# Performance work log

Measured on AMD Instinct MI355X. Metric: run time of the kernel, lower is better.

The kernel has to match this reference:

```python
import jax, jax.numpy as jnp
import numpy as np
import math

B, T1, T2, T3, D = 8, 32, 32, 16, 512
L, DL = 20, 128


def setup_inputs() -> dict:
    key = jax.random.key(0)
    ks = jax.random.split(key, 16)
    s = lambda fan: 1.0 / math.sqrt(fan)
    return {
        "f_c": jax.random.normal(ks[0], (B, T1, T2, T3, D), jnp.float32),
        "f_w": jax.random.normal(ks[1], (B, L, D), jnp.float32),
        "f_s": jax.random.normal(ks[2], (B, D), jnp.float32),
        "f_m": jax.random.normal(ks[3], (B, T1, T2, D), jnp.float32),
        "Wc_down": jax.random.normal(ks[4], (DL, D), jnp.float32) * s(D),
        "bc_down": jnp.zeros((DL,), jnp.float32),
        "Ww": jax.random.normal(ks[5], (DL, D), jnp.float32) * s(D),
        "bw": jnp.zeros((DL,), jnp.float32),
        "Ws": jax.random.normal(ks[6], (DL, D), jnp.float32) * s(D),
        "bs": jnp.zeros((DL,), jnp.float32),
        "Wq": jax.random.normal(ks[7], (DL, DL), jnp.float32) * s(DL),
        "bq": jnp.zeros((DL,), jnp.float32),
        "Wk": jax.random.normal(ks[8], (DL, DL), jnp.float32) * s(DL),
        "bk": jnp.zeros((DL,), jnp.float32),
        "Wc_up": jax.random.normal(ks[9], (D, DL), jnp.float32) * s(DL),
        "bc_up": jnp.zeros((D,), jnp.float32),
    }


def reference(f_c, f_w, f_s, f_m, Wc_down, bc_down, Ww, bw, Ws, bs,
              Wq, bq, Wk, bk, Wc_up, bc_up):
    inv_sqrt_dl = 1.0 / math.sqrt(DL)
    # 1x1 conv projections == per-position linear layers
    f_c_hat = jnp.einsum('bxyzd,ld->bxyzl', f_c, Wc_down) + bc_down  # [B,T1,T2,T3,dl]
    f_w_hat = f_w @ Ww.T + bw                                        # [B,L,dl]
    f_s_hat = f_s @ Ws.T + bs                                        # [B,dl]
    # Content attention: query from map, key/value from words
    q = f_c_hat @ Wq.T + bq                                          # [B,T1,T2,T3,dl]
    k = f_w_hat @ Wk.T + bk                                          # [B,L,dl]
    scores = jnp.einsum('bxyzd,bld->bxyzl', q, k) * inv_sqrt_dl
    attn = jax.nn.softmax(scores, axis=-1)
    f_caq = jnp.einsum('bxyzl,bld->bxyzd', attn, f_w_hat)            # [B,T1,T2,T3,dl]
    # Gate with sentence feature
    f_cq = f_c_hat * (f_caq + f_s_hat[:, None, None, None, :])
    # Self-attention over last spatial axis (T3)
    A_c = jnp.einsum('bxyzd,bxywd->bxyzw', f_cq, f_cq) * inv_sqrt_dl  # [B,T1,T2,T3,T3]
    A_c = jax.nn.softmax(A_c, axis=-1)
    f_cc_hat = jnp.einsum('bxyzw,bxywd->bxyzd', A_c, f_c_hat)
    f_cc = jnp.einsum('bxyzl,dl->bxyzd', f_cc_hat, Wc_up) + bc_up     # [B,T1,T2,T3,D]
    # Sigmoid gating residual for f_m
    g_m = jax.nn.sigmoid(f_m * f_s[:, None, None, :])
    fbar_m = g_m * f_m                                                # [B,T1,T2,D]
    return f_cc + f_c + fbar_m[:, :, :, None, :]
```

## Files before the change

### kernel.cpp

```cpp
#include <hip/hip_runtime.h>
#include <math.h>

#define B_ 8
#define T1_ 32
#define T2_ 32
#define T3_ 16
#define D_ 512
#define L_ 20
#define DL_ 128
#define M_ (B_*T1_*T2_*T3_)

#define WS_FW   0
#define WS_KQ   20480
#define WS_FS   40960
#define WS_SB   41984
#define WS_WDB  42144
#define WS_WUB  74912

typedef __attribute__((ext_vector_type(8))) short short8_t;
typedef __attribute__((ext_vector_type(4))) float f32x4;

__device__ __forceinline__ unsigned short f2b(float f) {
  unsigned int u = __float_as_uint(f);
  return (unsigned short)((u + 0x7fffu + ((u >> 16) & 1u)) >> 16);
}
__device__ __forceinline__ float b2f(short s) {
  return __uint_as_float(((unsigned)(unsigned short)s) << 16);
}
__device__ __forceinline__ int4 pack8(float4 a, float4 b) {
  int4 p;
  p.x = (int)f2b(a.x) | ((int)f2b(a.y) << 16);
  p.y = (int)f2b(a.z) | ((int)f2b(a.w) << 16);
  p.z = (int)f2b(b.x) | ((int)f2b(b.y) << 16);
  p.w = (int)f2b(b.z) | ((int)f2b(b.w) << 16);
  return p;
}

__global__ __launch_bounds__(256) void k0_convert(
    const float* __restrict__ Wd, const float* __restrict__ Wu,
    unsigned short* __restrict__ wdb, unsigned short* __restrict__ wub) {
  int g = blockIdx.x * 256 + threadIdx.x;
  if (g < 16384) {
    float4 v = ((const float4*)Wd)[g];
    ushort4 h; h.x = f2b(v.x); h.y = f2b(v.y); h.z = f2b(v.z); h.w = f2b(v.w);
    ((ushort4*)wdb)[g] = h;
  } else {
    int q = g - 16384;
    float4 v = ((const float4*)Wu)[q];
    ushort4 h; h.x = f2b(v.x); h.y = f2b(v.y); h.z = f2b(v.z); h.w = f2b(v.w);
    ((ushort4*)wub)[q] = h;
  }
}

__global__ __launch_bounds__(128) void k1_small(
    const float* __restrict__ f_w, const float* __restrict__ f_s,
    const float* __restrict__ Ww, const float* __restrict__ bw,
    const float* __restrict__ Ws, const float* __restrict__ bs,
    const float* __restrict__ Wq, const float* __restrict__ bq,
    const float* __restrict__ Wk, const float* __restrict__ bk,
    float* __restrict__ ws) {
  const int bl = blockIdx.x;
  const int b = bl / L_, l = bl % L_;
  const int d = threadIdx.x;
  __shared__ float s_fw[DL_];
  __shared__ float s_k[DL_];
  {
    const float* x = f_w + (size_t)(b*L_+l)*D_;
    const float* w = Ww + (size_t)d*D_;
    float acc = 0.f;
    for (int i = 0; i < D_; i += 4)
      acc += x[i]*w[i] + x[i+1]*w[i+1] + x[i+2]*w[i+2] + x[i+3]*w[i+3];
    acc += bw[d];
    s_fw[d] = acc;
    ws[WS_FW + (b*L_+l)*DL_ + d] = acc;
  }
  if (l == 0) {
    const float* x = f_s + (size_t)b*D_;
    const float* w = Ws + (size_t)d*D_;
    float acc = 0.f;
    for (int i = 0; i < D_; i += 4)
      acc += x[i]*w[i] + x[i+1]*w[i+1] + x[i+2]*w[i+2] + x[i+3]*w[i+3];
    ws[WS_FS + b*DL_ + d] = acc + bs[d];
  }
  __syncthreads();
  {
    const float* w = Wk + (size_t)d*DL_;
    float acc = 0.f;
    for (int i = 0; i < DL_; ++i) acc += s_fw[i]*w[i];
    s_k[d] = acc + bk[d];
  }
  __syncthreads();
  {
    float acc = 0.f;
    for (int c = 0; c < DL_; ++c) acc += s_k[c] * Wq[c*DL_ + d];
    ws[WS_KQ + (b*L_+l)*DL_ + d] = acc;
  }
  if (d == 0) {
    float acc = 0.f;
    for (int c = 0; c < DL_; ++c) acc += bq[c]*s_k[c];
    ws[WS_SB + b*L_ + l] = acc;
  }
}

#define SFCH_B 0
#define FCQ_B  8192
#define WD_B   16384
#define FC_B   32768
#define KQ_B   16384
#define FW_B   21824
#define FS_B   27264
#define SB_B   27776
#define ATTN_B 27904
#define AC_B   30592
#define WU_B   16384
#define SMEM_B 36864

__global__ __launch_bounds__(256, 4) void k2_fused(
    const float* __restrict__ f_c, const unsigned short* __restrict__ wdb,
    const unsigned short* __restrict__ wub,
    const float* __restrict__ bc_down, const float* __restrict__ bc_up,
    const float* __restrict__ f_m, const float* __restrict__ f_s,
    const float* __restrict__ ws, float* __restrict__ out) {
  __shared__ __align__(16) char smb[SMEM_B];
  float* sAttn = (float*)(smb + ATTN_B);
  float* sAc   = (float*)(smb + AC_B);
  float* sFs   = (float*)(smb + FS_B);
  float* sSb   = (float*)(smb + SB_B);

  const int t = threadIdx.x;
  const int row0 = blockIdx.x * 32;
  const int b = row0 >> 14;
  const int lane = t & 63, w = t >> 6;
  const int l15 = lane & 15, l4 = lane >> 4;
  const int wr = (w & 1) * 16;
  const int wc = w >> 1;
  const float inv_sqrt_dl = 0.08838834764831843f;
  const f32x4 z4 = {0.f, 0.f, 0.f, 0.f};
  const int sd_r = t >> 3, sd_k8 = (t & 7) * 8;

  f32x4 dacc[4];
  #pragma unroll
  for (int cf = 0; cf < 4; ++cf) dacc[cf] = z4;

  for (int kc = 0; kc < D_; kc += 64) {
    #pragma unroll
    for (int i = 0; i < 4; ++i) {
      int idx = t + i*256;
      int d = idx >> 3, kb = idx & 7;
      *(int4*)(smb + WD_B + d*128 + ((kb*16) ^ ((d & 7) << 4))) =
        *(const int4*)(wdb + (size_t)d*D_ + kc + kb*8);
    }
    {
      const float* src = f_c + (size_t)(row0 + sd_r)*D_ + kc + sd_k8;
      float4 v0 = *(const float4*)src;
      float4 v1 = *(const float4*)(src + 4);
      int4 pk = pack8(v0, v1);
      *(int4*)(smb + FC_B + sd_r*128 + ((sd_k8*2) ^ ((sd_r & 7) << 4))) = pk;
    }
    __syncthreads();
    #pragma unroll
    for (int ks = 0; ks < 2; ++ks) {
      const int rr = wr + l15;
      short8_t bfrag = *(const short8_t*)(smb + FC_B + rr*128 +
                        ((ks*64 + l4*16) ^ ((rr & 7) << 4)));
      #pragma unroll
      for (int cf = 0; cf < 4; ++cf) {
        const int d = wc*64 + cf*16 + l15;
        short8_t afrag = *(const short8_t*)(smb + WD_B + d*128 +
                          ((ks*64 + l4*16) ^ ((d & 7) << 4)));
        dacc[cf] = __builtin_amdgcn_mfma_f32_16x16x32_bf16(afrag, bfrag, dacc[cf], 0, 0, 0);
      }
    }
    __syncthreads();
  }
  {
    const int rr = wr + l15;
    const int rs = (rr & 7) << 4;
    #pragma unroll
    for (int cf = 0; cf < 4; ++cf) {
      const int d0 = wc*64 + cf*16 + l4*4;
      float4 bias = *(const float4*)(bc_down + d0);
      ushort4 pk;
      pk.x = f2b(dacc[cf][0] + bias.x); pk.y = f2b(dacc[cf][1] + bias.y);
      pk.z = f2b(dacc[cf][2] + bias.z); pk.w = f2b(dacc[cf][3] + bias.w);
      *(ushort4*)(smb + SFCH_B + rr*256 + ((d0*2) ^ rs)) = pk;
    }
  }
  for (int p = t; p < L_*16; p += 256) {
    const int l = p >> 4, c8 = (p & 15) * 8;
    float4 a0 = *(const float4*)(ws + WS_KQ + (b*L_+l)*DL_ + c8);
    float4 a1 = *(const float4*)(ws + WS_KQ + (b*L_+l)*DL_ + c8 + 4);
    *(int4*)(smb + KQ_B + l*272 + c8*2) = pack8(a0, a1);
    float4 b0 = *(const float4*)(ws + WS_FW + (b*L_+l)*DL_ + c8);
    float4 b1 = *(const float4*)(ws + WS_FW + (b*L_+l)*DL_ + c8 + 4);
    *(int4*)(smb + FW_B + l*272 + c8*2) = pack8(b0, b1);
  }
  if (t < 32) *(float4*)(sFs + t*4) = *(const float4*)(ws + WS_FS + b*DL_ + t*4);
  if (t < L_) sSb[t] = ws[WS_SB + b*L_ + t];
  __syncthreads();

  for (int p = t; p < 32*L_; p += 256) {
    const int r = p / L_, l = p - r*L_;
    const int qs = (r & 7) << 4;
    const char* qrow = smb + SFCH_B + r*256;
    const short* kr = (const short*)(smb + KQ_B + l*272);
    float s = 0.f;
    #pragma unroll
    for (int k = 0; k < DL_; k += 8) {
      short8_t qv = *(const short8_t*)(qrow + ((k*2) ^ qs));
      short8_t kv = *(const short8_t*)(kr + k);
      s += b2f(qv[0])*b2f(kv[0]) + b2f(qv[1])*b2f(kv[1])
         + b2f(qv[2])*b2f(kv[2]) + b2f(qv[3])*b2f(kv[3])
         + b2f(qv[4])*b2f(kv[4]) + b2f(qv[5])*b2f(kv[5])
         + b2f(qv[6])*b2f(kv[6]) + b2f(qv[7])*b2f(kv[7]);
    }
    sAttn[r*21 + l] = (s + sSb[l]) * inv_sqrt_dl;
  }
  __syncthreads();
  if (t < 32) {
    float* srow = sAttn + t*21;
    float m = -1e30f;
    for (int l = 0; l < L_; ++l) m = fmaxf(m, srow[l]);
    float sum = 0.f;
    for (int l = 0; l < L_; ++l) { float e = __expf(srow[l]-m); srow[l] = e; sum += e; }
    float inv = 1.f/sum;
    for (int l = 0; l < L_; ++l) srow[l] *= inv;
  }
  __syncthreads();
  for (int p = t; p < 1024; p += 256) {
    const int r = p >> 5, d4 = (p & 31) * 4;
    float ax = 0.f, ay = 0.f, az = 0.f, aw = 0.f;
    for (int l = 0; l < L_; ++l) {
      float a = sAttn[r*21 + l];
      ushort4 wv = *(const ushort4*)(smb + FW_B + l*272 + d4*2);
      ax += a*b2f((short)wv.x); ay += a*b2f((short)wv.y);
      az += a*b2f((short)wv.z); aw += a*b2f((short)wv.w);
    }
    const int rs = (r & 7) << 4;
    float4 fs4 = *(const float4*)(sFs + d4);
    ushort4 fh = *(const ushort4*)(smb + SFCH_B + r*256 + ((d4*2) ^ rs));
    ushort4 pk;
    pk.x = f2b(b2f((short)fh.x)*(ax+fs4.x));
    pk.y = f2b(b2f((short)fh.y)*(ay+fs4.y));
    pk.z = f2b(b2f((short)fh.z)*(az+fs4.z));
    pk.w = f2b(b2f((short)fh.w)*(aw+fs4.w));
    *(ushort4*)(smb + FCQ_B + r*256 + ((d4*2) ^ rs)) = pk;
  }
  __syncthreads();
  for (int p = t; p < 512; p += 256) {
    const int g = p >> 8, z = (p >> 4) & 15, wq = p & 15;
    const int xr = g*16 + z, yr = g*16 + wq;
    const char* xb = smb + FCQ_B + xr*256;
    const char* yb = smb + FCQ_B + yr*256;
    const int xs = (xr & 7) << 4, ys = (yr & 7) << 4;
    float s = 0.f;
    #pragma unroll
    for (int k = 0; k < DL_; k += 8) {
      short8_t xv = *(const short8_t*)(xb + ((k*2) ^ xs));
      short8_t yv = *(const short8_t*)(yb + ((k*2) ^ ys));
      s += b2f(xv[0])*b2f(yv[0]) + b2f(xv[1])*b2f(yv[1])
         + b2f(xv[2])*b2f(yv[2]) + b2f(xv[3])*b2f(yv[3])
         + b2f(xv[4])*b2f(yv[4]) + b2f(xv[5])*b2f(yv[5])
         + b2f(xv[6])*b2f(yv[6]) + b2f(xv[7])*b2f(yv[7]);
    }
    sAc[(g*16+z)*17 + wq] = s * inv_sqrt_dl;
  }
  __syncthreads();
  if (t < 32) {
    float* srow = sAc + t*17;
    float m = -1e30f;
    for (int wq = 0; wq < 16; ++wq) m = fmaxf(m, srow[wq]);
    float sum = 0.f;
    for (int wq = 0; wq < 16; ++wq) { float e = __expf(srow[wq]-m); srow[wq] = e; sum += e; }
    float inv = 1.f/sum;
    for (int wq = 0; wq < 16; ++wq) srow[wq] *= inv;
  }
  __syncthreads();
  for (int p = t; p < 1024; p += 256) {
    const int r = p >> 5, d4 = (p & 31)*4;
    const int g = r >> 4, z = r & 15;
    float ax = 0.f, ay = 0.f, az = 0.f, aw = 0.f;
    #pragma unroll
    for (int wq = 0; wq < 16; ++wq) {
      float a = sAc[(g*16+z)*17 + wq];
      const int fr = g*16 + wq;
      ushort4 fv = *(const ushort4*)(smb + SFCH_B + fr*256 + ((d4*2) ^ ((fr & 7) << 4)));
      ax += a*b2f((short)fv.x); ay += a*b2f((short)fv.y);
      az += a*b2f((short)fv.z); aw += a*b2f((short)fv.w);
    }
    ushort4 pk;
    pk.x = f2b(ax); pk.y = f2b(ay); pk.z = f2b(az); pk.w = f2b(aw);
    *(ushort4*)(smb + FCQ_B + r*256 + ((d4*2) ^ ((r & 7) << 4))) = pk;
  }
  __syncthreads();

  const int rr = wr + l15;
  const char* fcqrow = smb + FCQ_B + rr*256;
  const int xsw = (rr & 7) << 4;
  const int grow = row0 + rr;
  const size_t obase = (size_t)grow * D_;
  const size_t mbase = (size_t)(grow >> 4) * D_;
  for (int ch = 0; ch < 8; ++ch) {
    #pragma unroll
    for (int i = 0; i < 4; ++i) {
      int idx = t + i*256;
      int d = idx >> 4, kb = idx & 15;
      *(int4*)(smb + WU_B + d*256 + ((kb*16) ^ ((d & 7) << 4))) =
        *(const int4*)(wub + (size_t)(ch*64 + d)*DL_ + kb*8);
    }
    __syncthreads();
    f32x4 uacc[2]; uacc[0] = z4; uacc[1] = z4;
    #pragma unroll
    for (int ks = 0; ks < 4; ++ks) {
      short8_t bfrag = *(const short8_t*)(fcqrow + ((ks*64 + l4*16) ^ xsw));
      #pragma unroll
      for (int cf = 0; cf < 2; ++cf) {
        const int dd = wc*32 + cf*16 + l15;
        short8_t afrag = *(const short8_t*)(smb + WU_B + dd*256 +
                          ((ks*64 + l4*16) ^ ((dd & 7) << 4)));
        uacc[cf] = __builtin_amdgcn_mfma_f32_16x16x32_bf16(afrag, bfrag, uacc[cf], 0, 0, 0);
      }
    }
    #pragma unroll
    for (int cf = 0; cf < 2; ++cf) {
      const int d0 = ch*64 + wc*32 + cf*16 + l4*4;
      float4 bias = *(const float4*)(bc_up + d0);
      float4 fs4 = *(const float4*)(f_s + (size_t)b*D_ + d0);
      float4 fm4 = *(const float4*)(f_m + mbase + d0);
      float4 fc4 = *(const float4*)(f_c + obase + d0);
      float4 o;
      o.x = uacc[cf][0] + bias.x + fc4.x + fm4.x/(1.f + __expf(-fm4.x*fs4.x));
      o.y = uacc[cf][1] + bias.y + fc4.y + fm4.y/(1.f + __expf(-fm4.y*fs4.y));
      o.z = uacc[cf][2] + bias.z + fc4.z + fm4.z/(1.f + __expf(-fm4.z*fs4.z));
      o.w = uacc[cf][3] + bias.w + fc4.w + fm4.w/(1.f + __expf(-fm4.w*fs4.w));
      *(float4*)(out + obase + d0) = o;
    }
    __syncthreads();
  }
}

extern "C" void kernel_launch(void* const* d_in, const int* in_sizes, int n_in,
                              void* d_out, int out_size, void* d_ws, size_t ws_size,
                              hipStream_t stream) {
  (void)in_sizes; (void)n_in; (void)out_size; (void)ws_size;
  const float* f_c     = (const float*)d_in[0];
  const float* f_w     = (const float*)d_in[1];
  const float* f_s     = (const float*)d_in[2];
  const float* f_m     = (const float*)d_in[3];
  const float* Wc_down = (const float*)d_in[4];
  const float* bc_down = (const float*)d_in[5];
  const float* Ww      = (const float*)d_in[6];
  const float* bw      = (const float*)d_in[7];
  const float* Ws      = (const float*)d_in[8];
  const float* bs      = (const float*)d_in[9];
  const float* Wq      = (const float*)d_in[10];
  const float* bq      = (const float*)d_in[11];
  const float* Wk      = (const float*)d_in[12];
  const float* bk      = (const float*)d_in[13];
  const float* Wc_up   = (const float*)d_in[14];
  const float* bc_up   = (const float*)d_in[15];
  float* out = (float*)d_out;
  float* wsf = (float*)d_ws;
  unsigned short* wdb = (unsigned short*)(wsf + WS_WDB);
  unsigned short* wub = (unsigned short*)(wsf + WS_WUB);

  hipLaunchKernelGGL(k0_convert, dim3(128), dim3(256), 0, stream,
                     Wc_down, Wc_up, wdb, wub);
  hipLaunchKernelGGL(k1_small, dim3(B_*L_), dim3(128), 0, stream,
                     f_w, f_s, Ww, bw, Ws, bs, Wq, bq, Wk, bk, wsf);
  hipLaunchKernelGGL(k2_fused, dim3(M_/32), dim3(256), 0, stream,
                     f_c, wdb, wub, bc_down, bc_up, f_m, f_s, wsf, out);
}
```

Before: 269.6 us.

## Move attention score, context and self-attention matmuls onto MFMA with register softmax

Replaces the scalar bf16 dot-product loops for query-word scores, attention-weighted word aggregation, and the T3 self-attention scores with MFMA 16x16x32 bf16 instructions. The K and transposed word-feature tiles are zero-padded to 32 rows and stored in swizzled LDS layouts. The self-attention softmax now runs in registers with lane shuffles instead of a serial 32-thread pass. It also adds a bf16 quantization of the attention probabilities and uses more shared memory, which could affect accuracy and occupancy.

```diff
diff --git a/kernel.cpp b/kernel.cpp
--- a/kernel.cpp
+++ b/kernel.cpp
@@ -107,13 +107,14 @@
 #define WD_B   16384
 #define FC_B   32768
 #define KQ_B   16384
-#define FW_B   21824
-#define FS_B   27264
-#define SB_B   27776
-#define ATTN_B 27904
-#define AC_B   30592
+#define FWT_B  24576
+#define ATB_B  32768
+#define FS_B   36864
+#define SB_B   37376
+#define ATTN_B 37504
+#define AC_B   37504
 #define WU_B   16384
-#define SMEM_B 36864
+#define SMEM_B 40960
 
 __global__ __launch_bounds__(256, 4) void k2_fused(
     const float* __restrict__ f_c, const unsigned short* __restrict__ wdb,
@@ -186,35 +187,54 @@
       *(ushort4*)(smb + SFCH_B + rr*256 + ((d0*2) ^ rs)) = pk;
     }
   }
-  for (int p = t; p < L_*16; p += 256) {
-    const int l = p >> 4, c8 = (p & 15) * 8;
-    float4 a0 = *(const float4*)(ws + WS_KQ + (b*L_+l)*DL_ + c8);
-    float4 a1 = *(const float4*)(ws + WS_KQ + (b*L_+l)*DL_ + c8 + 4);
-    *(int4*)(smb + KQ_B + l*272 + c8*2) = pack8(a0, a1);
-    float4 b0 = *(const float4*)(ws + WS_FW + (b*L_+l)*DL_ + c8);
-    float4 b1 = *(const float4*)(ws + WS_FW + (b*L_+l)*DL_ + c8 + 4);
-    *(int4*)(smb + FW_B + l*272 + c8*2) = pack8(b0, b1);
+  for (int p = t; p < 32*16; p += 256) {
+    const int l = p >> 4, k8 = (p & 15) * 8;
+    int4 v = {0,0,0,0};
+    if (l < L_) {
+      float4 a0 = *(const float4*)(ws + WS_KQ + (b*L_+l)*DL_ + k8);
+      float4 a1 = *(const float4*)(ws + WS_KQ + (b*L_+l)*DL_ + k8 + 4);
+      v = pack8(a0, a1);
+    }
+    *(int4*)(smb + KQ_B + l*256 + ((k8*2) ^ ((l & 7) << 4))) = v;
+  }
+  for (int p = t; p < 512; p += 256) {
+    const int d = p >> 2, l8 = (p & 3) * 8;
+    float vv[8];
+    #pragma unroll
+    for (int e = 0; e < 8; ++e) {
+      const int l = l8 + e;
+      vv[e] = (l < L_) ? ws[WS_FW + (b*L_+l)*DL_ + d] : 0.f;
+    }
+    int4 v;
+    v.x = (int)f2b(vv[0]) | ((int)f2b(vv[1]) << 16);
+    v.y = (int)f2b(vv[2]) | ((int)f2b(vv[3]) << 16);
+    v.z = (int)f2b(vv[4]) | ((int)f2b(vv[5]) << 16);
+    v.w = (int)f2b(vv[6]) | ((int)f2b(vv[7]) << 16);
+    *(int4*)(smb + FWT_B + d*64 + ((l8*2) ^ ((d & 3) << 4))) = v;
   }
   if (t < 32) *(float4*)(sFs + t*4) = *(const float4*)(ws + WS_FS + b*DL_ + t*4);
   if (t < L_) sSb[t] = ws[WS_SB + b*L_ + t];
   __syncthreads();
 
-  for (int p = t; p < 32*L_; p += 256) {
-    const int r = p / L_, l = p - r*L_;
-    const int qs = (r & 7) << 4;
-    const char* qrow = smb + SFCH_B + r*256;
-    const short* kr = (const short*)(smb + KQ_B + l*272);
-    float s = 0.f;
-    #pragma unroll
-    for (int k = 0; k < DL_; k += 8) {
-      short8_t qv = *(const short8_t*)(qrow + ((k*2) ^ qs));
-      short8_t kv = *(const short8_t*)(kr + k);
-      s += b2f(qv[0])*b2f(kv[0]) + b2f(qv[1])*b2f(kv[1])
-         + b2f(qv[2])*b2f(kv[2]) + b2f(qv[3])*b2f(kv[3])
-         + b2f(qv[4])*b2f(kv[4]) + b2f(qv[5])*b2f(kv[5])
-         + b2f(qv[6])*b2f(kv[6]) + b2f(qv[7])*b2f(kv[7]);
-    }
-    sAttn[r*21 + l] = (s + sSb[l]) * inv_sqrt_dl;
+  {
+    const int lt = w & 1, rt = w >> 1;
+    const int arow = lt*16 + l15;
+    const int brow = rt*16 + l15;
+    f32x4 sacc = z4;
+    #pragma unroll
+    for (int ks = 0; ks < 4; ++ks) {
+      short8_t af = *(const short8_t*)(smb + KQ_B + arow*256 +
+                     ((ks*64 + l4*16) ^ ((arow & 7) << 4)));
+      short8_t bf = *(const short8_t*)(smb + SFCH_B + brow*256 +
+                     ((ks*64 + l4*16) ^ ((brow & 7) << 4)));
+      sacc = __builtin_amdgcn_mfma_f32_16x16x32_bf16(af, bf, sacc, 0, 0, 0);
+    }
+    const int r2 = rt*16 + l15;
+    #pragma unroll
+    for (int reg = 0; reg < 4; ++reg) {
+      const int lval = lt*16 + l4*4 + reg;
+      if (lval < L_) sAttn[r2*21 + lval] = (sacc[reg] + sSb[lval]) * inv_sqrt_dl;
+    }
   }
   __syncthreads();
   if (t < 32) {
@@ -227,53 +247,87 @@
     for (int l = 0; l < L_; ++l) srow[l] *= inv;
   }
   __syncthreads();
-  for (int p = t; p < 1024; p += 256) {
-    const int r = p >> 5, d4 = (p & 31) * 4;
-    float ax = 0.f, ay = 0.f, az = 0.f, aw = 0.f;
-    for (int l = 0; l < L_; ++l) {
-      float a = sAttn[r*21 + l];
-      ushort4 wv = *(const ushort4*)(smb + FW_B + l*272 + d4*2);
-      ax += a*b2f((short)wv.x); ay += a*b2f((short)wv.y);
-      az += a*b2f((short)wv.z); aw += a*b2f((short)wv.w);
-    }
-    const int rs = (r & 7) << 4;
-    float4 fs4 = *(const float4*)(sFs + d4);
-    ushort4 fh = *(const ushort4*)(smb + SFCH_B + r*256 + ((d4*2) ^ rs));
-    ushort4 pk;
-    pk.x = f2b(b2f((short)fh.x)*(ax+fs4.x));
-    pk.y = f2b(b2f((short)fh.y)*(ay+fs4.y));
-    pk.z = f2b(b2f((short)fh.z)*(az+fs4.z));
-    pk.w = f2b(b2f((short)fh.w)*(aw+fs4.w));
-    *(ushort4*)(smb + FCQ_B + r*256 + ((d4*2) ^ rs)) = pk;
-  }
-  __syncthreads();
-  for (int p = t; p < 512; p += 256) {
-    const int g = p >> 8, z = (p >> 4) & 15, wq = p & 15;
-    const int xr = g*16 + z, yr = g*16 + wq;
-    const char* xb = smb + FCQ_B + xr*256;
-    const char* yb = smb + FCQ_B + yr*256;
-    const int xs = (xr & 7) << 4, ys = (yr & 7) << 4;
-    float s = 0.f;
-    #pragma unroll
-    for (int k = 0; k < DL_; k += 8) {
-      short8_t xv = *(const short8_t*)(xb + ((k*2) ^ xs));
-      short8_t yv = *(const short8_t*)(yb + ((k*2) ^ ys));
-      s += b2f(xv[0])*b2f(yv[0]) + b2f(xv[1])*b2f(yv[1])
-         + b2f(xv[2])*b2f(yv[2]) + b2f(xv[3])*b2f(yv[3])
-         + b2f(xv[4])*b2f(yv[4]) + b2f(xv[5])*b2f(yv[5])
-         + b2f(xv[6])*b2f(yv[6]) + b2f(xv[7])*b2f(yv[7]);
-    }
-    sAc[(g*16+z)*17 + wq] = s * inv_sqrt_dl;
-  }
-  __syncthreads();
-  if (t < 32) {
-    float* srow = sAc + t*17;
-    float m = -1e30f;
-    for (int wq = 0; wq < 16; ++wq) m = fmaxf(m, srow[wq]);
-    float sum = 0.f;
-    for (int wq = 0; wq < 16; ++wq) { float e = __expf(srow[wq]-m); srow[wq] = e; sum += e; }
-    float inv = 1.f/sum;
-    for (int wq = 0; wq < 16; ++wq) srow[wq] *= inv;
+  {
+    const int r = t >> 3, k8 = (t & 7) * 8;
+    int4 v = {0,0,0,0};
+    if (k8 < L_) {
+      float vv[8];
+      #pragma unroll
+      for (int e = 0; e < 8; ++e) {
+        const int l = k8 + e;
+        vv[e] = (l < L_) ? sAttn[r*21 + l] : 0.f;
+      }
+      v.x = (int)f2b(vv[0]) | ((int)f2b(vv[1]) << 16);
+      v.y = (int)f2b(vv[2]) | ((int)f2b(vv[3]) << 16);
+      v.z = (int)f2b(vv[4]) | ((int)f2b(vv[5]) << 16);
+      v.w = (int)f2b(vv[6]) | ((int)f2b(vv[7]) << 16);
+    }
+    *(int4*)(smb + ATB_B + r*128 + ((k8*2) ^ ((r & 7) << 4))) = v;
+  }
+  __syncthreads();
+  {
+    f32x4 cacc[2][2];
+    cacc[0][0] = z4; cacc[0][1] = z4; cacc[1][0] = z4; cacc[1][1] = z4;
+    #pragma unroll
+    for (int dt = 0; dt < 2; ++dt) {
+      const int arow = (w*2 + dt)*16 + l15;
+      short8_t af = *(const short8_t*)(smb + FWT_B + arow*64 +
+                     ((l4*16) ^ ((arow & 3) << 4)));
+      #pragma unroll
+      for (int rt = 0; rt < 2; ++rt) {
+        const int brow = rt*16 + l15;
+        short8_t bf = *(const short8_t*)(smb + ATB_B + brow*128 +
+                       ((l4*16) ^ ((brow & 7) << 4)));
+        cacc[dt][rt] = __builtin_amdgcn_mfma_f32_16x16x32_bf16(af, bf, cacc[dt][rt], 0, 0, 0);
+      }
+    }
+    #pragma unroll
+    for (int dt = 0; dt < 2; ++dt)
+    #pragma unroll
+    for (int rt = 0; rt < 2; ++rt) {
+      const int d0 = (w*2 + dt)*16 + l4*4;
+      const int r = rt*16 + l15;
+      const int rs = (r & 7) << 4;
+      float4 fs4 = *(const float4*)(sFs + d0);
+      ushort4 fh = *(const ushort4*)(smb + SFCH_B + r*256 + ((d0*2) ^ rs));
+      ushort4 pk;
+      pk.x = f2b(b2f((short)fh.x)*(cacc[dt][rt][0] + fs4.x));
+      pk.y = f2b(b2f((short)fh.y)*(cacc[dt][rt][1] + fs4.y));
+      pk.z = f2b(b2f((short)fh.z)*(cacc[dt][rt][2] + fs4.z));
+      pk.w = f2b(b2f((short)fh.w)*(cacc[dt][rt][3] + fs4.w));
+      *(ushort4*)(smb + FCQ_B + r*256 + ((d0*2) ^ rs)) = pk;
+    }
+  }
+  __syncthreads();
+  if (w < 2) {
+    const int zrow = w*16 + l15;
+    f32x4 pacc = z4;
+    #pragma unroll
+    for (int ks = 0; ks < 4; ++ks) {
+      short8_t fq = *(const short8_t*)(smb + FCQ_B + zrow*256 +
+                     ((ks*64 + l4*16) ^ ((zrow & 7) << 4)));
+      pacc = __builtin_amdgcn_mfma_f32_16x16x32_bf16(fq, fq, pacc, 0, 0, 0);
+    }
+    float p0[4], m[4], e[4], s[4];
+    #pragma unroll
+    for (int reg = 0; reg < 4; ++reg) p0[reg] = pacc[reg] * inv_sqrt_dl;
+    #pragma unroll
+    for (int reg = 0; reg < 4; ++reg) {
+      m[reg] = p0[reg];
+      m[reg] = fmaxf(m[reg], __shfl_xor(m[reg], 1));
+      m[reg] = fmaxf(m[reg], __shfl_xor(m[reg], 2));
+      m[reg] = fmaxf(m[reg], __shfl_xor(m[reg], 4));
+      m[reg] = fmaxf(m[reg], __shfl_xor(m[reg], 8));
+      e[reg] = __expf(p0[reg] - m[reg]);
+      s[reg] = e[reg];
+      s[reg] += __shfl_xor(s[reg], 1);
+      s[reg] += __shfl_xor(s[reg], 2);
+      s[reg] += __shfl_xor(s[reg], 4);
+      s[reg] += __shfl_xor(s[reg], 8);
+    }
+    #pragma unroll
+    for (int reg = 0; reg < 4; ++reg)
+      sAc[(w*16 + l4*4 + reg)*17 + l15] = e[reg] / s[reg];
   }
   __syncthreads();
   for (int p = t; p < 1024; p += 256) {
```

New measurement: 252.9 us. -6.2%, faster.
